# Kernel optimization log

Measured on AMD Instinct MI355X. Metric: run time of the kernel, lower is better.

## Reference

```python
import jax, jax.numpy as jnp
import numpy as np

ALPHA = 1.0
BETA = 1.0
N, D, C = 131072, 512, 1000


def setup_inputs() -> dict:
    key = jax.random.key(0)
    k1, k2, k3 = jax.random.split(key, 3)
    feat = jax.random.normal(k1, (N, D), dtype=jnp.float32)
    classifier = jax.random.normal(k2, (C, D), dtype=jnp.float32)
    target = jax.random.randint(k3, (N,), 0, C, dtype=jnp.int64)
    return {"feat": feat, "classifier": classifier, "target": target}


def reference(feat, classifier, target):
    # --- weight-wise MHE term ---
    w = classifier / jnp.linalg.norm(classifier, axis=1, keepdims=True)  # [C, D]
    sq = jnp.sum(w * w, axis=1)  # [C]
    d2 = jnp.maximum(sq[:, None] + sq[None, :] - 2.0 * (w @ w.T), 0.0)  # [C, C] squared dists
    # triu(diagonal=1) then mask >0  <=>  upper-triangular strictly positive entries
    triu = jnp.triu(jnp.ones((C, C), dtype=bool), k=1)
    mask = triu & (d2 > 0)
    safe_d2 = jnp.where(mask, d2, 1.0)
    # mean of 1/d^2 over masked entries (1/(d*d) == 1/d2)
    weight_wise = jnp.sum(jnp.where(mask, 1.0 / safe_d2, 0.0)) / jnp.sum(mask)

    # --- sample-wise concentration term (per-class mean of dist to its weight) ---
    feat_n = feat / jnp.linalg.norm(feat, axis=1, keepdims=True)  # [N, D]
    w_t = jax.lax.stop_gradient(w)[target]  # [N, D], class mean detached
    dist = jnp.linalg.norm(feat_n - w_t, axis=1)  # [N] cdist to a single point
    counts = jax.ops.segment_sum(jnp.ones_like(dist), target, num_segments=C)  # [C]
    sums = jax.ops.segment_sum(dist, target, num_segments=C)  # [C]
    present = counts > 0
    class_means = jnp.where(present, sums / jnp.maximum(counts, 1.0), 0.0)
    sample_wise_all = jnp.sum(class_means) / jnp.sum(present)

    return (sample_wise_all * BETA, weight_wise * ALPHA, feat)
```

## Files before the change

### kernel.cpp

```cpp
#include <hip/hip_runtime.h>

#define NN 131072
#define DD 512
#define CC 1000

#define CT 64
#define KCP 32
#define NTILE 16
#define NPAIR 136
#define SROWS 8
#define NSAMP (NN / SROWS)

typedef float f32x4 __attribute__((ext_vector_type(4)));
typedef float f32x2 __attribute__((ext_vector_type(2)));


__device__ __forceinline__ float wave_reduce(float v) {
#pragma unroll
    for (int m = 32; m > 0; m >>= 1) v += __shfl_xor(v, m, 64);
    return v;
}

__global__ __launch_bounds__(64) void knorm(const float* __restrict__ cls,
                                            float* __restrict__ w,
                                            float* __restrict__ sqw) {
    int c = blockIdx.x;
    int lane = threadIdx.x;
    const float4* src = (const float4*)(cls + (size_t)c * DD) + lane * 2;
    float4 f0 = src[0], f1 = src[1];
    float s = f0.x * f0.x + f0.y * f0.y + f0.z * f0.z + f0.w * f0.w +
              f1.x * f1.x + f1.y * f1.y + f1.z * f1.z + f1.w * f1.w;
    s = wave_reduce(s);
    float inv = rsqrtf(s);
    float4 w0 = make_float4(f0.x * inv, f0.y * inv, f0.z * inv, f0.w * inv);
    float4 w1 = make_float4(f1.x * inv, f1.y * inv, f1.z * inv, f1.w * inv);
    float q = w0.x * w0.x + w0.y * w0.y + w0.z * w0.z + w0.w * w0.w +
              w1.x * w1.x + w1.y * w1.y + w1.z * w1.z + w1.w * w1.w;
    q = wave_reduce(q);
    float4* dst = (float4*)(w + (size_t)c * DD) + lane * 2;
    dst[0] = w0;
    dst[1] = w1;
    if (lane == 0) sqw[c] = q;
}

__global__ __launch_bounds__(256) void kmain(const float* __restrict__ feat,
                                             const int* __restrict__ target,
                                             const float* __restrict__ w,
                                             const float* __restrict__ sqw,
                                             float* __restrict__ class_sum,
                                             float* __restrict__ class_cnt,
                                             float* __restrict__ pair_acc,
                                             float* __restrict__ out_feat) {
    int t = threadIdx.x;

    if (blockIdx.x < NPAIR) {
        __shared__ float As[KCP][CT + 4];
        __shared__ float Bs[KCP][CT + 4];
        __shared__ float rs[4], rc[4];

        int bi = 0, rem = blockIdx.x;
        while (rem >= NTILE - bi) { rem -= NTILE - bi; ++bi; }
        int bj = bi + rem;
        int i0 = bi * CT, j0 = bj * CT;

        int tx = t & 15, ty = t >> 4;
        int lrow = t >> 2;
        int kc = (t & 3) * 8;

        float acc[4][4] = {{0.f, 0.f, 0.f, 0.f}};

        for (int k0 = 0; k0 < DD; k0 += KCP) {
            f32x4 a0 = {0.f, 0.f, 0.f, 0.f}, a1 = a0, b0 = a0, b1 = a0;
            int gi = i0 + lrow, gj = j0 + lrow;
            if (gi < CC) {
                const f32x4* p = (const f32x4*)(w + (size_t)gi * DD + k0 + kc);
                a0 = p[0]; a1 = p[1];
            }
            if (gj < CC) {
                const f32x4* p = (const f32x4*)(w + (size_t)gj * DD + k0 + kc);
                b0 = p[0]; b1 = p[1];
            }
            __syncthreads();
            As[kc + 0][lrow] = a0.x; As[kc + 1][lrow] = a0.y;
            As[kc + 2][lrow] = a0.z; As[kc + 3][lrow] = a0.w;
            As[kc + 4][lrow] = a1.x; As[kc + 5][lrow] = a1.y;
            As[kc + 6][lrow] = a1.z; As[kc + 7][lrow] = a1.w;
            Bs[kc + 0][lrow] = b0.x; Bs[kc + 1][lrow] = b0.y;
            Bs[kc + 2][lrow] = b0.z; Bs[kc + 3][lrow] = b0.w;
            Bs[kc + 4][lrow] = b1.x; Bs[kc + 5][lrow] = b1.y;
            Bs[kc + 6][lrow] = b1.z; Bs[kc + 7][lrow] = b1.w;
            __syncthreads();
#pragma unroll
            for (int k = 0; k < KCP; ++k) {
                f32x4 av = *(const f32x4*)&As[k][4 * ty];
                f32x4 bv = *(const f32x4*)&Bs[k][4 * tx];
#pragma unroll
                for (int a = 0; a < 4; ++a)
#pragma unroll
                    for (int b = 0; b < 4; ++b)
                        acc[a][b] += av[a] * bv[b];
            }
        }

        float lsum = 0.f, lcnt = 0.f;
        int ib = i0 + 4 * ty, jb = j0 + 4 * tx;
#pragma unroll
        for (int a = 0; a < 4; ++a)
#pragma unroll
            for (int b = 0; b < 4; ++b) {
                int i = ib + a, j = jb + b;
                if (j > i && j < CC) {
                    float d2 = sqw[i] + sqw[j] - 2.f * acc[a][b];
                    if (d2 > 0.f) { lsum += 1.f / d2; lcnt += 1.f; }
                }
            }
        lsum = wave_reduce(lsum);
        lcnt = wave_reduce(lcnt);
        int wv = t >> 6;
        if ((t & 63) == 0) { rs[wv] = lsum; rc[wv] = lcnt; }
        __syncthreads();
        if (t == 0) {
            atomicAdd(pair_acc + 0, rs[0] + rs[1] + rs[2] + rs[3]);
            atomicAdd(pair_acc + 1, rc[0] + rc[1] + rc[2] + rc[3]);
        }
        return;
    }

    __shared__ float red[8][4][2];
    long long n0 = (long long)(blockIdx.x - NPAIR) * SROWS;
    int col4 = t & 127;
    int rhalf = t >> 7;

    const f32x4* f4 = (const f32x4*)feat;
    const f32x4* w4 = (const f32x4*)w;
    f32x2* o2 = (f32x2*)out_feat;

    int tg[4];
#pragma unroll
    for (int i = 0; i < 4; ++i) tg[i] = target[n0 + rhalf + 2 * i];

    size_t fi[4];
    f32x4 f[4];
#pragma unroll
    for (int i = 0; i < 4; ++i) {
        fi[i] = (size_t)(n0 + rhalf + 2 * i) * 128 + col4;
        f[i] = __builtin_nontemporal_load(f4 + fi[i]);
    }

    f32x4 wv[4];
#pragma unroll
    for (int i = 0; i < 4; ++i) wv[i] = w4[(size_t)tg[i] * 128 + col4];

#pragma unroll
    for (int i = 0; i < 4; ++i) {
        f32x2 lo = {f[i].x, f[i].y}, hi = {f[i].z, f[i].w};
        __builtin_nontemporal_store(lo, o2 + 2 * fi[i]);
        __builtin_nontemporal_store(hi, o2 + 2 * fi[i] + 1);
    }

    float ff[4], fw[4];
#pragma unroll
    for (int i = 0; i < 4; ++i) {
        ff[i] = f[i].x * f[i].x + f[i].y * f[i].y + f[i].z * f[i].z + f[i].w * f[i].w;
        fw[i] = f[i].x * wv[i].x + f[i].y * wv[i].y + f[i].z * wv[i].z + f[i].w * wv[i].w;
    }
#pragma unroll
    for (int m = 16; m > 0; m >>= 1)
#pragma unroll
        for (int i = 0; i < 4; ++i) {
            ff[i] += __shfl_xor(ff[i], m, 64);
            fw[i] += __shfl_xor(fw[i], m, 64);
        }
    int p = t >> 5;
    if ((t & 31) == 0) {
#pragma unroll
        for (int i = 0; i < 4; ++i) { red[p][i][0] = ff[i]; red[p][i][1] = fw[i]; }
    }
    __syncthreads();
    if ((t & 127) < 4) {
        int i = t & 127;
        int base = rhalf * 4;
        float sff = red[base][i][0] + red[base + 1][i][0] +
                    red[base + 2][i][0] + red[base + 3][i][0];
        float sfw = red[base][i][1] + red[base + 1][i][1] +
                    red[base + 2][i][1] + red[base + 3][i][1];
        int tgt = tg[i];
        float inv = rsqrtf(sff);
        float d2 = sff * inv * inv + sqw[tgt] - 2.f * inv * sfw;
        d2 = fmaxf(d2, 0.f);
        atomicAdd(class_sum + tgt, sqrtf(d2));
        atomicAdd(class_cnt + tgt, 1.f);
    }
}

__global__ __launch_bounds__(256) void kfin(const float* __restrict__ class_sum,
                                            const float* __restrict__ class_cnt,
                                            const float* __restrict__ pair_acc,
                                            float* __restrict__ out) {
    float msum = 0.f, pcnt = 0.f;
    for (int c = threadIdx.x; c < CC; c += 256) {
        float cnt = class_cnt[c];
        if (cnt > 0.f) {
            msum += class_sum[c] / cnt;
            pcnt += 1.f;
        }
    }
    msum = wave_reduce(msum);
    pcnt = wave_reduce(pcnt);
    __shared__ float rs[4], rc[4];
    int wv = threadIdx.x >> 6;
    if ((threadIdx.x & 63) == 0) { rs[wv] = msum; rc[wv] = pcnt; }
    __syncthreads();
    if (threadIdx.x == 0) {
        float sm = rs[0] + rs[1] + rs[2] + rs[3];
        float sp = rc[0] + rc[1] + rc[2] + rc[3];
        out[0] = 1.0f * (sm / sp);
        out[1] = 1.0f * (pair_acc[0] / pair_acc[1]);
    }
}

extern "C" void kernel_launch(void* const* d_in, const int* in_sizes, int n_in,
                              void* d_out, int out_size, void* d_ws, size_t ws_size,
                              hipStream_t stream) {
    const float* feat = (const float*)d_in[0];
    const float* cls = (const float*)d_in[1];
    const int* target = (const int*)d_in[2];
    float* out = (float*)d_out;
    float* ws = (float*)d_ws;

    float* w = ws;
    float* sqw = ws + 512000;
    float* class_sum = ws + 513000;
    float* class_cnt = ws + 514000;
    float* pair_acc = ws + 515000;

    hipMemsetAsync(class_sum, 0, (2 * CC + 2) * sizeof(float), stream);

    knorm<<<CC, 64, 0, stream>>>(cls, w, sqw);
    kmain<<<NPAIR + NSAMP, 256, 0, stream>>>(feat, target, w, sqw,
                                             class_sum, class_cnt, pair_acc, out + 2);
    kfin<<<1, 256, 0, stream>>>(class_sum, class_cnt, pair_acc, out);
}
```

Measured before the change: 498.7 us.

## Process rows per wavefront and realign output stores with cross-lane shuffles

The per-sample path now gives each 64-lane wavefront two whole rows, so the norm and dot reductions use only wave shuffles and no shared memory or block barrier. The feature copy to the output, which was split into two 8-byte stores per lane (the output starts 2 floats off 16-byte alignment), now shuffles neighbour values so most lanes issue one aligned 16-byte store. The aim is fewer, wider store transactions and less synchronisation on this bandwidth-bound copy. The cost is extra shuffles and some edge-case store branches.

```diff
diff --git a/kernel.cpp b/kernel.cpp
--- a/kernel.cpp
+++ b/kernel.cpp
@@ -19,6 +19,10 @@
 #pragma unroll
     for (int m = 32; m > 0; m >>= 1) v += __shfl_xor(v, m, 64);
     return v;
+}
+
+__device__ __forceinline__ float dot4(f32x4 a, f32x4 b) {
+    return a.x * b.x + a.y * b.y + a.z * b.z + a.w * b.w;
 }
 
 __global__ __launch_bounds__(64) void knorm(const float* __restrict__ cls,
@@ -43,6 +47,27 @@
     if (lane == 0) sqw[c] = q;
 }
 
+__device__ __forceinline__ void store_row(float* __restrict__ orow, int lane,
+                                          f32x4 v0, f32x4 v1) {
+    int nl = (lane + 1) & 63;
+    float s0x = __shfl(v0.x, nl, 64), s0y = __shfl(v0.y, nl, 64);
+    float s1x = __shfl(v1.x, nl, 64), s1y = __shfl(v1.y, nl, 64);
+    bool last = (lane == 63);
+    f32x4 st1 = {v0.z, v0.w, last ? s1x : s0x, last ? s1y : s0y};
+    __builtin_nontemporal_store(st1, (f32x4*)(orow + 2 + 4 * lane));
+    if (!last) {
+        f32x4 st2 = {v1.z, v1.w, s1x, s1y};
+        __builtin_nontemporal_store(st2, (f32x4*)(orow + 258 + 4 * lane));
+    } else {
+        f32x2 tl = {v1.z, v1.w};
+        __builtin_nontemporal_store(tl, (f32x2*)(orow + 510));
+    }
+    if (lane == 0) {
+        f32x2 hd = {v0.x, v0.y};
+        __builtin_nontemporal_store(hd, (f32x2*)(orow + 0));
+    }
+}
+
 __global__ __launch_bounds__(256) void kmain(const float* __restrict__ feat,
                                              const int* __restrict__ target,
                                              const float* __restrict__ w,
@@ -126,70 +151,56 @@
         return;
     }
 
-    __shared__ float red[8][4][2];
-    long long n0 = (long long)(blockIdx.x - NPAIR) * SROWS;
-    int col4 = t & 127;
-    int rhalf = t >> 7;
+    int lane = t & 63;
+    long long gw = (long long)(blockIdx.x - NPAIR) * 4 + (t >> 6);
+    long long r0 = gw * 2;
 
     const f32x4* f4 = (const f32x4*)feat;
     const f32x4* w4 = (const f32x4*)w;
-    f32x2* o2 = (f32x2*)out_feat;
-
-    int tg[4];
-#pragma unroll
-    for (int i = 0; i < 4; ++i) tg[i] = target[n0 + rhalf + 2 * i];
-
-    size_t fi[4];
-    f32x4 f[4];
-#pragma unroll
-    for (int i = 0; i < 4; ++i) {
-        fi[i] = (size_t)(n0 + rhalf + 2 * i) * 128 + col4;
-        f[i] = __builtin_nontemporal_load(f4 + fi[i]);
-    }
-
-    f32x4 wv[4];
-#pragma unroll
-    for (int i = 0; i < 4; ++i) wv[i] = w4[(size_t)tg[i] * 128 + col4];
-
-#pragma unroll
-    for (int i = 0; i < 4; ++i) {
-        f32x2 lo = {f[i].x, f[i].y}, hi = {f[i].z, f[i].w};
-        __builtin_nontemporal_store(lo, o2 + 2 * fi[i]);
-        __builtin_nontemporal_store(hi, o2 + 2 * fi[i] + 1);
-    }
-
-    float ff[4], fw[4];
-#pragma unroll
-    for (int i = 0; i < 4; ++i) {
-        ff[i] = f[i].x * f[i].x + f[i].y * f[i].y + f[i].z * f[i].z + f[i].w * f[i].w;
-        fw[i] = f[i].x * wv[i].x + f[i].y * wv[i].y + f[i].z * wv[i].z + f[i].w * wv[i].w;
-    }
-#pragma unroll
-    for (int m = 16; m > 0; m >>= 1)
-#pragma unroll
-        for (int i = 0; i < 4; ++i) {
-            ff[i] += __shfl_xor(ff[i], m, 64);
-            fw[i] += __shfl_xor(fw[i], m, 64);
-        }
-    int p = t >> 5;
-    if ((t & 31) == 0) {
-#pragma unroll
-        for (int i = 0; i < 4; ++i) { red[p][i][0] = ff[i]; red[p][i][1] = fw[i]; }
-    }
-    __syncthreads();
-    if ((t & 127) < 4) {
-        int i = t & 127;
-        int base = rhalf * 4;
-        float sff = red[base][i][0] + red[base + 1][i][0] +
-                    red[base + 2][i][0] + red[base + 3][i][0];
-        float sfw = red[base][i][1] + red[base + 1][i][1] +
-                    red[base + 2][i][1] + red[base + 3][i][1];
-        int tgt = tg[i];
-        float inv = rsqrtf(sff);
-        float d2 = sff * inv * inv + sqw[tgt] - 2.f * inv * sfw;
+
+    int tg0 = target[r0];
+    int tg1 = target[r0 + 1];
+
+    size_t fb = (size_t)r0 * 128 + lane;
+    f32x4 a0 = __builtin_nontemporal_load(f4 + fb);
+    f32x4 a1 = __builtin_nontemporal_load(f4 + fb + 64);
+    f32x4 b0 = __builtin_nontemporal_load(f4 + fb + 128);
+    f32x4 b1 = __builtin_nontemporal_load(f4 + fb + 192);
+
+    f32x4 u0 = w4[(size_t)tg0 * 128 + lane];
+    f32x4 u1 = w4[(size_t)tg0 * 128 + 64 + lane];
+    f32x4 v0 = w4[(size_t)tg1 * 128 + lane];
+    f32x4 v1 = w4[(size_t)tg1 * 128 + 64 + lane];
+
+    float* orow0 = out_feat + (size_t)r0 * 512;
+    store_row(orow0, lane, a0, a1);
+    store_row(orow0 + 512, lane, b0, b1);
+
+    float ff0 = dot4(a0, a0) + dot4(a1, a1);
+    float fw0 = dot4(a0, u0) + dot4(a1, u1);
+    float ff1 = dot4(b0, b0) + dot4(b1, b1);
+    float fw1 = dot4(b0, v0) + dot4(b1, v1);
+
+#pragma unroll
+    for (int m = 32; m > 0; m >>= 1) {
+        ff0 += __shfl_xor(ff0, m, 64);
+        fw0 += __shfl_xor(fw0, m, 64);
+        ff1 += __shfl_xor(ff1, m, 64);
+        fw1 += __shfl_xor(fw1, m, 64);
+    }
+
+    if (lane == 0) {
+        float inv = rsqrtf(ff0);
+        float d2 = ff0 * inv * inv + sqw[tg0] - 2.f * inv * fw0;
         d2 = fmaxf(d2, 0.f);
-        atomicAdd(class_sum + tgt, sqrtf(d2));
-        atomicAdd(class_cnt + tgt, 1.f);
+        atomicAdd(class_sum + tg0, sqrtf(d2));
+        atomicAdd(class_cnt + tg0, 1.f);
+    } else if (lane == 1) {
+        float inv = rsqrtf(ff1);
+        float d2 = ff1 * inv * inv + sqw[tg1] - 2.f * inv * fw1;
+        d2 = fmaxf(d2, 0.f);
+        atomicAdd(class_sum + tg1, sqrtf(d2));
+        atomicAdd(class_cnt + tg1, 1.f);
     }
 }
 
```

Measured after the change: 498.4 us. Within noise of the previous version (-0.1%).
